# Performance work log

Measured on AMD Instinct MI355X. Metric: run time of the kernel, lower is better.

Reference implementation:

```python
import jax, jax.numpy as jnp
import numpy as np

B, D, K, A = 32768, 256, 1024, 32
MIN_LOG_STD, MAX_LOG_STD = -20.0, 2.0


def setup_inputs() -> dict:
    key = jax.random.key(0)
    ks = jax.random.split(key, 9)
    return {
        "obs": jax.random.normal(ks[0], (B, D), dtype=jnp.float32),
        "mean_C": jax.random.normal(ks[1], (K, D), dtype=jnp.float32),
        "mean_sigma": jnp.abs(jax.random.normal(ks[2], (K,), dtype=jnp.float32)) + 0.1,
        "mean_w": jax.random.normal(ks[3], (A, K), dtype=jnp.float32),
        "mean_b": jax.random.normal(ks[4], (A,), dtype=jnp.float32),
        "std_C": jax.random.normal(ks[5], (K, D), dtype=jnp.float32),
        "std_sigma": jnp.abs(jax.random.normal(ks[6], (K,), dtype=jnp.float32)) + 0.1,
        "std_w": jax.random.normal(ks[7], (A, K), dtype=jnp.float32),
        "std_b": jax.random.normal(ks[8], (A,), dtype=jnp.float32),
    }


def _rbf(x, C, sigma_sq, w, b):
    # r[b,k] = sum_d (x[b,d] - C[k,d])^2, expanded to avoid a [B,K,D] intermediate
    x2 = jnp.sum(x * x, axis=-1, keepdims=True)           # [B,1]
    c2 = jnp.sum(C * C, axis=-1)[None, :]                  # [1,K]
    r = x2 - 2.0 * (x @ C.T) + c2                          # [B,K]
    phi = jnp.exp(-r / (2.0 * jnp.abs(sigma_sq)[None, :]))  # [B,K]
    return phi @ w.T + b[None, :]                          # [B,A]


def reference(obs, mean_C, mean_sigma, mean_w, mean_b,
              std_C, std_sigma, std_w, std_b):
    action_mean = _rbf(obs, mean_C, mean_sigma, mean_w, mean_b)
    std_raw = _rbf(obs, std_C, std_sigma, std_w, std_b)
    action_std = jnp.exp(jnp.clip(std_raw, MIN_LOG_STD, MAX_LOG_STD))
    return jnp.concatenate((action_mean, action_std), axis=-1)  # [B, 2A]
```

## Files before the change

### kernel.cpp

```cpp
#include <hip/hip_runtime.h>


typedef float floatx4 __attribute__((ext_vector_type(4)));
typedef int   intx4  __attribute__((ext_vector_type(4)));
typedef unsigned int u32;
typedef unsigned char u8;

constexpr float LOG2E = 1.4426950408889634f;
constexpr float QS    = 25.4f;
constexpr float SINV2 = (5.0f / 127.0f) * (5.0f / 127.0f);

__device__ __forceinline__ u32 pk_fp8(float a, float b, float c, float d) {
  u32 v = __builtin_amdgcn_cvt_pk_fp8_f32(a, b, 0u, 0);
  v = __builtin_amdgcn_cvt_pk_fp8_f32(c, d, v, 1);
  return v;
}
__device__ __forceinline__ long mk64(u32 lo, u32 hi) {
  return (long)lo | ((long)hi << 32);
}
__device__ __forceinline__ int q8(float x) {
  return (int)rintf(fminf(fmaxf(x * QS, -127.f), 127.f));
}
__device__ __forceinline__ u32 pk_i8(int a, int b, int c, int d) {
  return (u32)(a & 255) | ((u32)(b & 255) << 8) | ((u32)(c & 255) << 16) | ((u32)(d & 255) << 24);
}

__global__ void prep(const float* __restrict__ mC, const float* __restrict__ mS,
                     const float* __restrict__ sC, const float* __restrict__ sS,
                     const float* __restrict__ mw, const float* __restrict__ sw,
                     const float* __restrict__ obs,
                     u8* __restrict__ Cb2, float* __restrict__ a2g,
                     float* __restrict__ g2n, u8* __restrict__ wt,
                     u8* __restrict__ qb, float* __restrict__ hx2f)
{
  const int blk = blockIdx.x;
  if (blk < 512) {
    const int wq = threadIdx.x >> 6;
    const int t  = threadIdx.x & 63;
    const int b  = blk * 4 + wq;
    const int half = b >> 10;
    const int k = b & 1023;
    const float* src = (half ? sC : mC) + (size_t)k * 256;
    float4 f = *(const float4*)(src + t * 4);
    int i0 = q8(f.x), i1 = q8(f.y), i2 = q8(f.z), i3 = q8(f.w);
    const int ct = b >> 6, row = b & 63;
    const int wvv = row >> 4, cc = row & 15;
    const int ks = t >> 4, qq = (t >> 2) & 3, j0 = (t & 3) * 4;
    *(u32*)(Cb2 + (size_t)ct * 16384 + wvv * 4096 + (ks * 64 + qq * 16 + cc) * 16 + j0) =
        pk_i8(i0, i1, i2, i3);
    int is = i0 * i0 + i1 * i1 + i2 * i2 + i3 * i3;
    for (int off = 32; off > 0; off >>= 1) is += __shfl_down(is, off, 64);
    if (t == 0) {
      float sig = fabsf((half ? sS : mS)[k]);
      float t2 = SINV2 * LOG2E * 0.5f / sig;
      a2g[b] = 2.f * t2;
      g2n[b] = -t2 * (float)is;
    }
  } else if (blk < 528) {
    const int m   = blk - 512;
    const int tid = threadIdx.x;
    const int wv  = tid >> 6;
    const int lane = tid & 63;
    const int c   = lane & 15;
    const int q   = lane >> 4;
    const int kbE = ((2 * m) & 15) * 64 + 16 * wv + 4 * q;
    const float* src = (m < 8) ? mw : sw;
    float4 f00 = *(const float4*)(src + (size_t)c * 1024 + kbE);
    float4 f01 = *(const float4*)(src + (size_t)c * 1024 + kbE + 64);
    float4 f10 = *(const float4*)(src + (size_t)(16 + c) * 1024 + kbE);
    float4 f11 = *(const float4*)(src + (size_t)(16 + c) * 1024 + kbE + 64);
    uint4 o;
    o.x = pk_fp8(f00.x, f00.y, f00.z, f00.w);
    o.y = pk_fp8(f01.x, f01.y, f01.z, f01.w);
    o.z = pk_fp8(f10.x, f10.y, f10.z, f10.w);
    o.w = pk_fp8(f11.x, f11.y, f11.z, f11.w);
    *(uint4*)(wt + ((size_t)m * 256 + tid) * 16) = o;
  } else {
    const int wq = threadIdx.x >> 6;
    const int t  = threadIdx.x & 63;
    const int row = (blk - 528) * 4 + wq;
    float4 f = *(const float4*)(obs + (size_t)row * 256 + t * 4);
    int i0 = q8(f.x), i1 = q8(f.y), i2 = q8(f.z), i3 = q8(f.w);
    const int T = row >> 4, c = row & 15;
    const int ks = t >> 4, q = (t >> 2) & 3, j0 = (t & 3) * 4;
    *(u32*)(qb + (size_t)T * 4096 + ks * 1024 + q * 256 + c * 16 + j0) =
        pk_i8(i0, i1, i2, i3);
    int is = i0 * i0 + i1 * i1 + i2 * i2 + i3 * i3;
    for (int off = 32; off > 0; off >>= 1) is += __shfl_down(is, off, 64);
    if (t == 0) hx2f[row] = 0.5f * (float)is;
  }
}

__global__ __launch_bounds__(256, 4)
void policy_main(const u8* __restrict__ qb,
                 const float* __restrict__ hx2f,
                 const u8* __restrict__ Cb2,
                 const float* __restrict__ a2g,
                 const float* __restrict__ g2n,
                 const u8* __restrict__ wt,
                 const float* __restrict__ mbias,
                 const float* __restrict__ sbias,
                 float* __restrict__ out)
{
  __shared__ __align__(16) float red[4608];

  const int tid  = threadIdx.x;
  const int lane = tid & 63;
  const int wv   = tid >> 6;
  const int c    = lane & 15;
  const int q    = lane >> 4;
  const int half = blockIdx.x & 1;
  const int row0 = (blockIdx.x >> 1) * 32;
  const int kslc = 16 * wv + 4 * q;
  const int cfo  = wv * 4096 + lane * 16;

  const u8*    cbh = Cb2 + (size_t)half * (16 * 16384);
  const float* a2h = a2g + half * 1024;
  const float* g2h = g2n + half * 1024;
  const u8*    wtl = wt + (size_t)half * 32768 + (size_t)tid * 16;

#define LOADCF(CF, t)                                                     \
  { const u8* g0_ = cbh + (size_t)(t) * 16384 + cfo;                      \
    CF[0] = *(const intx4*)(g0_);                                         \
    CF[1] = *(const intx4*)(g0_ + 1024);                                  \
    CF[2] = *(const intx4*)(g0_ + 2048);                                  \
    CF[3] = *(const intx4*)(g0_ + 3072); }

  intx4 cfU[4], cfV[4];
  LOADCF(cfU, 0)
  LOADCF(cfV, 1)

  intx4 ob[2][4];
  {
    const u8* qrow = qb + (size_t)(row0 >> 4) * 4096 + lane * 16;
    #pragma unroll
    for (int nt = 0; nt < 2; ++nt)
      #pragma unroll
      for (int ks = 0; ks < 4; ++ks)
        ob[nt][ks] = *(const intx4*)(qrow + nt * 4096 + ks * 1024);
  }

  float hx2[2];
  hx2[0] = hx2f[row0 + c];
  hx2[1] = hx2f[row0 + 16 + c];

  const intx4 Z4i = {0, 0, 0, 0};
  const floatx4 Z4 = {0.f, 0.f, 0.f, 0.f};
  floatx4 acc[2][2];
  #pragma unroll
  for (int a2i = 0; a2i < 2; ++a2i)
    #pragma unroll
    for (int nt = 0; nt < 2; ++nt) acc[a2i][nt] = Z4;

  intx4 a1E[2], a1O[2];
  u32 pE[2], pc[2];

#define GEMM1PAIR()                                                             \
  { _Pragma("unroll")                                                           \
    for (int nt = 0; nt < 2; ++nt) {                                            \
      a1E[nt] = __builtin_amdgcn_mfma_i32_16x16x64_i8(cfU[0], ob[nt][0], Z4i, 0, 0, 0); \
      a1O[nt] = __builtin_amdgcn_mfma_i32_16x16x64_i8(cfV[0], ob[nt][0], Z4i, 0, 0, 0); \
    }                                                                           \
    _Pragma("unroll")                                                           \
    for (int ks = 1; ks < 4; ++ks) {                                            \
      _Pragma("unroll")                                                         \
      for (int nt = 0; nt < 2; ++nt) {                                          \
        a1E[nt] = __builtin_amdgcn_mfma_i32_16x16x64_i8(cfU[ks], ob[nt][ks], a1E[nt], 0, 0, 0); \
        a1O[nt] = __builtin_amdgcn_mfma_i32_16x16x64_i8(cfV[ks], ob[nt][ks], a1O[nt], 0, 0, 0); \
      }                                                                         \
    } }

#define EXPP(A1, AC, GC, DST)                                                   \
  { _Pragma("unroll")                                                           \
    for (int nt = 0; nt < 2; ++nt) {                                            \
      float t0 = (float)A1[nt][0] - hx2[nt], t1 = (float)A1[nt][1] - hx2[nt];   \
      float t2 = (float)A1[nt][2] - hx2[nt], t3 = (float)A1[nt][3] - hx2[nt];   \
      DST[nt] = pk_fp8(__builtin_amdgcn_exp2f(fmaf(AC.x, t0, GC.x)),            \
                       __builtin_amdgcn_exp2f(fmaf(AC.y, t1, GC.y)),            \
                       __builtin_amdgcn_exp2f(fmaf(AC.z, t2, GC.z)),            \
                       __builtin_amdgcn_exp2f(fmaf(AC.w, t3, GC.w))); } }

#define GEMM2P(WV4)                                                             \
  { long wA0 = mk64(WV4.x, WV4.y), wA1 = mk64(WV4.z, WV4.w);                    \
    _Pragma("unroll")                                                           \
    for (int nt = 0; nt < 2; ++nt) {                                            \
      long pb = mk64(pE[nt], pc[nt]);                                           \
      acc[0][nt] = __builtin_amdgcn_mfma_f32_16x16x32_fp8_fp8(wA0, pb, acc[0][nt], 0, 0, 0); \
      acc[1][nt] = __builtin_amdgcn_mfma_f32_16x16x32_fp8_fp8(wA1, pb, acc[1][nt], 0, 0, 0); \
    } }

#define STEP(mm, PF)                                                            \
  {                                                                             \
    uint4 wv4 = *(const uint4*)(wtl + (size_t)(mm) * 4096);                     \
    float4 acE = *(const float4*)(a2h + (2 * (mm)) * 64 + kslc);                \
    float4 gcE = *(const float4*)(g2h + (2 * (mm)) * 64 + kslc);                \
    float4 acO = *(const float4*)(a2h + (2 * (mm) + 1) * 64 + kslc);            \
    float4 gcO = *(const float4*)(g2h + (2 * (mm) + 1) * 64 + kslc);            \
    GEMM1PAIR()                                                                 \
    if (PF) { LOADCF(cfU, 2 * (mm) + 2) LOADCF(cfV, 2 * (mm) + 3) }             \
    EXPP(a1E, acE, gcE, pE)                                                     \
    EXPP(a1O, acO, gcO, pc)                                                     \
    GEMM2P(wv4)                                                                 \
  }

  #pragma unroll
  for (int mm = 0; mm < 7; ++mm) STEP(mm, 1)
  STEP(7, 0)
#undef STEP
#undef GEMM1PAIR
#undef EXPP
#undef GEMM2P
#undef LOADCF

  {
    float* myr = red + wv * 1152;
    #pragma unroll
    for (int a2i = 0; a2i < 2; ++a2i)
      #pragma unroll
      for (int nt = 0; nt < 2; ++nt)
        *(floatx4*)(myr + (nt * 16 + c) * 36 + a2i * 16 + 4 * q) = acc[a2i][nt];
  }
  __syncthreads();

  const float* bias = half ? sbias : mbias;
  #pragma unroll
  for (int i = 0; i < 4; ++i) {
    int idx = tid + 256 * i;
    int a = idx & 31;
    int b = idx >> 5;
    float v = red[b * 36 + a] + red[1152 + b * 36 + a] +
              red[2304 + b * 36 + a] + red[3456 + b * 36 + a];
    v += bias[a];
    if (half) {
      v = fminf(fmaxf(v, -20.f), 2.f);
      v = __builtin_amdgcn_exp2f(v * LOG2E);
    }
    out[(size_t)(row0 + b) * 64 + half * 32 + a] = v;
  }
}

extern "C" void kernel_launch(void* const* d_in, const int* in_sizes, int n_in,
                              void* d_out, int out_size, void* d_ws, size_t ws_size,
                              hipStream_t stream) {
  const float* obs = (const float*)d_in[0];
  const float* mC  = (const float*)d_in[1];
  const float* mS  = (const float*)d_in[2];
  const float* mW  = (const float*)d_in[3];
  const float* mB  = (const float*)d_in[4];
  const float* sC  = (const float*)d_in[5];
  const float* sS  = (const float*)d_in[6];
  const float* sW  = (const float*)d_in[7];
  const float* sB  = (const float*)d_in[8];
  float* out = (float*)d_out;

  u8*    Cb2  = (u8*)d_ws;
  float* a2g  = (float*)((char*)d_ws + 524288);
  float* g2n  = a2g + 2048;
  u8*    wt   = (u8*)(g2n + 2048);
  u8*    qb   = (u8*)d_ws + 655360;
  float* hx2f = (float*)((char*)d_ws + 655360 + 8388608);

  prep<<<8720, 256, 0, stream>>>(mC, mS, sC, sS, mW, sW, obs, Cb2, a2g, g2n, wt, qb, hx2f);
  policy_main<<<2048, 256, 0, stream>>>(qb, hx2f, Cb2, a2g, g2n, wt, mB, sB, out);
}
```

Measured before the change: 122.5 us.

## Software-pipeline GEMM1 one step ahead of exp and GEMM2

Restructures the main K loop so the first-stage MFMA for step mm+1 is issued before the exp/fp8-pack and second-stage MFMA of step mm. Weights and scale vectors for the next step are also loaded one iteration early. The aim is to hide MFMA latency behind the transcendental VALU work and overlap loads, at the cost of keeping extra accumulator copies live, which raises register pressure and may lower occupancy.

```diff
diff --git a/kernel.cpp b/kernel.cpp
--- a/kernel.cpp
+++ b/kernel.cpp
@@ -189,24 +189,44 @@
       acc[1][nt] = __builtin_amdgcn_mfma_f32_16x16x32_fp8_fp8(wA1, pb, acc[1][nt], 0, 0, 0); \
     } }
 
-#define STEP(mm, PF)                                                            \
-  {                                                                             \
-    uint4 wv4 = *(const uint4*)(wtl + (size_t)(mm) * 4096);                     \
-    float4 acE = *(const float4*)(a2h + (2 * (mm)) * 64 + kslc);                \
-    float4 gcE = *(const float4*)(g2h + (2 * (mm)) * 64 + kslc);                \
-    float4 acO = *(const float4*)(a2h + (2 * (mm) + 1) * 64 + kslc);            \
-    float4 gcO = *(const float4*)(g2h + (2 * (mm) + 1) * 64 + kslc);            \
-    GEMM1PAIR()                                                                 \
-    if (PF) { LOADCF(cfU, 2 * (mm) + 2) LOADCF(cfV, 2 * (mm) + 3) }             \
-    EXPP(a1E, acE, gcE, pE)                                                     \
-    EXPP(a1O, acO, gcO, pc)                                                     \
-    GEMM2P(wv4)                                                                 \
-  }
+  uint4  wv4c = *(const uint4*)(wtl);
+  float4 acEc = *(const float4*)(a2h + kslc);
+  float4 gcEc = *(const float4*)(g2h + kslc);
+  float4 acOc = *(const float4*)(a2h + 64 + kslc);
+  float4 gcOc = *(const float4*)(g2h + 64 + kslc);
+
+  GEMM1PAIR()
+  LOADCF(cfU, 2) LOADCF(cfV, 3)
 
   #pragma unroll
-  for (int mm = 0; mm < 7; ++mm) STEP(mm, 1)
-  STEP(7, 0)
-#undef STEP
+  for (int mm = 0; mm < 8; ++mm) {
+    intx4 s1E[2], s1O[2];
+    s1E[0] = a1E[0]; s1E[1] = a1E[1];
+    s1O[0] = a1O[0]; s1O[1] = a1O[1];
+
+    uint4  wv4n = wv4c;
+    float4 acEn = acEc, gcEn = gcEc, acOn = acOc, gcOn = gcOc;
+    if (mm < 7) {
+      wv4n = *(const uint4*)(wtl + (size_t)(mm + 1) * 4096);
+      acEn = *(const float4*)(a2h + (2 * (mm + 1)) * 64 + kslc);
+      gcEn = *(const float4*)(g2h + (2 * (mm + 1)) * 64 + kslc);
+      acOn = *(const float4*)(a2h + (2 * (mm + 1) + 1) * 64 + kslc);
+      gcOn = *(const float4*)(g2h + (2 * (mm + 1) + 1) * 64 + kslc);
+    }
+
+    if (mm < 7) {
+      GEMM1PAIR()
+    }
+    if (mm < 6) {
+      LOADCF(cfU, 2 * (mm + 2)) LOADCF(cfV, 2 * (mm + 2) + 1)
+    }
+
+    EXPP(s1E, acEc, gcEc, pE)
+    EXPP(s1O, acOc, gcOc, pc)
+    GEMM2P(wv4c)
+
+    wv4c = wv4n; acEc = acEn; gcEc = gcEn; acOc = acOn; gcOc = gcOn;
+  }
 #undef GEMM1PAIR
 #undef EXPP
 #undef GEMM2P
```

Measured after the change: 123.5 us. About the same (+0.9%).
